# Kernel tuning notes

Measured on AMD Instinct MI355X. Metric: run time of the kernel, lower is better.

Reference implementation:

```python
import jax, jax.numpy as jnp
import numpy as np

# V:N:M sparsity config (n=2 kept of m=8 per vector-block; mask pattern [1,0,1,0,0,0,0,0])
M_BLK = 8
KEEP_OFFSETS = np.array([0, 2], dtype=np.int32)  # positions kept in each m-block
B, S, D_IN, D_OUT = 2, 8192, 4096, 4096
K_KEPT = D_IN // M_BLK * len(KEEP_OFFSETS)  # 1024


def _keep_idx():
    # column indices of the surviving weight entries (same for every output row)
    blocks = np.arange(D_IN // M_BLK, dtype=np.int32)[:, None] * M_BLK  # [D_IN/M,1]
    return jnp.asarray((blocks + KEEP_OFFSETS[None, :]).reshape(-1))   # [K_KEPT]


def setup_inputs() -> dict:
    key = jax.random.key(0)
    k1, k2, k3 = jax.random.split(key, 3)
    x = jax.random.normal(k1, (B, S, D_IN), dtype=jnp.float32)
    values = jax.random.normal(k2, (D_OUT, K_KEPT), dtype=jnp.float32) * 0.02
    bias = jax.random.normal(k3, (D_OUT,), dtype=jnp.float32) * 0.02
    return {"x": x, "values": values, "bias": bias}


def reference(x, values, bias):
    # Sparse SpMM: gather kept input features, dense GEMM with compressed values.
    # Equivalent to x @ (masked dense W).T + bias, without materializing W.
    keep = _keep_idx()               # [K_KEPT] int32, constant metadata
    xg = x[..., keep]                # [B,S,K_KEPT]
    out = jnp.einsum('bsk,nk->bsn', xg, values) + bias  # [B,S,D_OUT]
    return out
```

## Files before the change

### kernel.cpp

```cpp
#include <hip/hip_runtime.h>
#include <hip/hip_bf16.h>


#define M_TOTAL 16384
#define DIN     4096
#define KDIM    1024
#define NDIM    4096

typedef unsigned short u16;
typedef unsigned int   u32;
typedef __bf16 bf16x8 __attribute__((ext_vector_type(8)));
typedef float  f32x4  __attribute__((ext_vector_type(4)));

typedef const void __attribute__((address_space(1)))* gp_t;
typedef void __attribute__((address_space(3)))*       lp_t;

__device__ __forceinline__ u16 f2bf(float f) {
    u32 u = __float_as_uint(f);
    u += 0x7FFFu + ((u >> 16) & 1u);
    return (u16)(u >> 16);
}
__device__ __forceinline__ u32 pack2(float a, float b) {
    return (u32)f2bf(a) | ((u32)f2bf(b) << 16);
}

__global__ void prep_kernel(const float* __restrict__ x, uint2* __restrict__ xg2,
                            const float* __restrict__ vals, uint4* __restrict__ vb4) {
    const int tid = threadIdx.x;
    if (blockIdx.x < 4096) {
        int i = blockIdx.x * 256 + tid;
        const int stride = 4096 * 256;
#pragma unroll
        for (int it = 0; it < 4; ++it, i += stride) {
            const f32x4* p = (const f32x4*)(x + (size_t)i * 16);
            f32x4 f0 = __builtin_nontemporal_load(p);
            f32x4 f1 = __builtin_nontemporal_load(p + 2);
            xg2[i] = make_uint2(pack2(f0.x, f0.z), pack2(f1.x, f1.z));
        }
    } else {
        const int i = (blockIdx.x - 4096) * 256 + tid;
        const f32x4* p = (const f32x4*)(vals + (size_t)i * 8);
        f32x4 a = __builtin_nontemporal_load(p);
        f32x4 b = __builtin_nontemporal_load(p + 1);
        vb4[i] = make_uint4(pack2(a.x, a.y), pack2(a.z, a.w),
                            pack2(b.x, b.y), pack2(b.z, b.w));
    }
}


#define LDSA(d, kh) (((d) * 2 + (kh)) * 16384)
#define LDSB(d, kh) (65536 + ((d) * 2 + (kh)) * 16384)

#define LOADA(d, kh, mh) { _Pragma("unroll") \
    for (int m_ = 0; m_ < 4; ++m_) \
        af[m_] = *(const bf16x8*)(lds + LDSA(d, kh) + (wr * 8 + (mh) * 4 + m_) * 1024 + fl_off); }

#define LOADB(d, kh) { _Pragma("unroll") \
    for (int n_ = 0; n_ < 4; ++n_) \
        bfr[n_] = *(const bf16x8*)(lds + LDSB(d, kh) + (wc * 4 + n_) * 1024 + fl_off); }

#define MFMA16(mh) { \
    __builtin_amdgcn_s_setprio(1); \
    _Pragma("unroll") for (int m_ = 0; m_ < 4; ++m_) \
    _Pragma("unroll") for (int n_ = 0; n_ < 4; ++n_) \
        acc[(mh) * 4 + m_][n_] = __builtin_amdgcn_mfma_f32_16x16x32_bf16( \
            af[m_], bfr[n_], acc[(mh) * 4 + m_][n_], 0, 0, 0); \
    __builtin_amdgcn_s_setprio(0); }

#define BAR() __builtin_amdgcn_s_barrier()
#define VMCNT6() asm volatile("s_waitcnt vmcnt(6)" ::: "memory")

__global__ __launch_bounds__(512, 2) void gemm_kernel(
    const u16* __restrict__ A, const u16* __restrict__ Bv,
    const float* __restrict__ bias, float* __restrict__ C)
{
    __shared__ __align__(1024) char lds[131072];

    const int tid  = threadIdx.x;
    const int lane = tid & 63;
    const int wid  = tid >> 6;
    const int wr   = wid >> 2;
    const int wc   = wid & 3;
    const int lrow = lane & 15;
    const int lg   = lane >> 4;

    const int bb   = blockIdx.x;
    const int btm0 = (bb & 7) * 8 + (bb >> 7);
    const int btn  = (bb >> 3) & 15;

    const int st_r0 = wid * 16 + (lane >> 2);
    const int st_ck = ((lane & 3) * 8) ^ ((lane & 32) >> 1);
    const u16* A0  = A  + (size_t)(btm0 * 256 + st_r0) * KDIM + st_ck;
    const u16* Bs0 = Bv + (size_t)(btn  * 256 + st_r0) * KDIM + st_ck;
    const int dst0 = tid * 16;

    const int fl_off = lrow * 64 + ((lg * 16) ^ (((lrow >> 3) & 1) << 5));

    auto STAGE = [&](const u16* as_, int s) {
        const int kt = s >> 2, j = s & 3;
        const int d = kt & 1, kh = (j >> 1) & 1;
        const int ko = kt * 64 + kh * 32;
        const u16* src = (j & 1) ? Bs0 : as_;
        const int base = ((j & 1) ? 65536 : 0) + (d * 2 + kh) * 16384;
        __builtin_amdgcn_global_load_lds((gp_t)(src + ko),
            (lp_t)(lds + base + dst0), 16, 0, 0);
        __builtin_amdgcn_global_load_lds((gp_t)(src + 128 * KDIM + ko),
            (lp_t)(lds + base + 8192 + dst0), 16, 0, 0);
    };

    const int c_col0 = btn * 256 + wc * 64 + lrow;
    float bvr[4];
#pragma unroll
    for (int n = 0; n < 4; ++n) bvr[n] = bias[c_col0 + n * 16];

    f32x4 acc[8][4] = {};
    bf16x8 af[4], bfr[4];

    STAGE(A0, 0); STAGE(A0, 1); STAGE(A0, 2); STAGE(A0, 3);
    STAGE(A0, 4); STAGE(A0, 5); STAGE(A0, 6);
    VMCNT6();
    BAR();

#pragma unroll 1
    for (int r = 0; r < 4; ++r) {
        const u16* Ar = A0 + (size_t)r * 512 * KDIM;
        const u16* An = (r < 3) ? (Ar + 512 * KDIM) : Ar;

#pragma unroll 1
        for (int t = 0; t < 7; ++t) {
            const int s0 = 8 * t + 7;
            LOADB(0, 0); LOADA(0, 0, 0); STAGE(Ar, s0);     BAR(); MFMA16(0); BAR();
            LOADA(0, 0, 1);              STAGE(Ar, s0 + 1); BAR(); MFMA16(1); BAR();
            LOADB(0, 1); LOADA(0, 1, 0); STAGE(Ar, s0 + 2); BAR(); MFMA16(0); BAR();
            LOADA(0, 1, 1);              STAGE(Ar, s0 + 3); BAR(); MFMA16(1);
            VMCNT6(); BAR();
            LOADB(1, 0); LOADA(1, 0, 0); STAGE(Ar, s0 + 4); BAR(); MFMA16(0); BAR();
            LOADA(1, 0, 1);              STAGE(Ar, s0 + 5); BAR(); MFMA16(1); BAR();
            LOADB(1, 1); LOADA(1, 1, 0); STAGE(Ar, s0 + 6); BAR(); MFMA16(0); BAR();
            LOADA(1, 1, 1);              STAGE(Ar, s0 + 7); BAR(); MFMA16(1);
            VMCNT6(); BAR();
        }
        LOADB(0, 0); LOADA(0, 0, 0); STAGE(Ar, 63); BAR(); MFMA16(0); BAR();
        LOADA(0, 0, 1);              STAGE(An, 0);  BAR(); MFMA16(1); BAR();
        LOADB(0, 1); LOADA(0, 1, 0); STAGE(An, 1);  BAR(); MFMA16(0); BAR();
        LOADA(0, 1, 1);              STAGE(An, 2);  BAR(); MFMA16(1);
        VMCNT6(); BAR();
        LOADB(1, 0); LOADA(1, 0, 0); STAGE(An, 3);  BAR(); MFMA16(0); BAR();
        LOADA(1, 0, 1);              STAGE(An, 4);  BAR(); MFMA16(1); BAR();
        LOADB(1, 1); LOADA(1, 1, 0); STAGE(An, 5);  BAR(); MFMA16(0); BAR();
        LOADA(1, 1, 1);              STAGE(An, 6);  BAR(); MFMA16(1);
        VMCNT6(); BAR();

        const int c_row0 = (btm0 + 2 * r) * 256 + wr * 128 + lg * 4;
#pragma unroll
        for (int mi = 0; mi < 8; ++mi) {
            const int row = c_row0 + (mi >> 2) * 64 + (mi & 3) * 16;
#pragma unroll
            for (int n = 0; n < 4; ++n) {
#pragma unroll
                for (int j = 0; j < 4; ++j)
                    __builtin_nontemporal_store(acc[mi][n][j] + bvr[n],
                        &C[(size_t)(row + j) * NDIM + c_col0 + n * 16]);
                acc[mi][n] = (f32x4){0.f, 0.f, 0.f, 0.f};
            }
        }
    }
}

extern "C" void kernel_launch(void* const* d_in, const int* in_sizes, int n_in,
                              void* d_out, int out_size, void* d_ws, size_t ws_size,
                              hipStream_t stream) {
    const float* x      = (const float*)d_in[0];
    const float* values = (const float*)d_in[1];
    const float* bias   = (const float*)d_in[2];
    float* out = (float*)d_out;

    u16* xg = (u16*)d_ws;
    u16* vb = (u16*)((char*)d_ws + ((size_t)32 << 20));

    prep_kernel<<<6144, 256, 0, stream>>>(x, (uint2*)xg, values, (uint4*)vb);
    gemm_kernel<<<256, 512, 0, stream>>>(xg, vb, bias, out);
}
```

Measured before the change: 212.4 us.

## Restructure GEMM main loop into per-phase wait/barrier pipeline

Reorganizes the GEMM K-loop so each phase first waits on outstanding global-to-LDS loads (vmcnt 10) and then hits a single barrier before issuing the next stage and the LDS fragment reads. This replaces the previous pattern of two barriers per phase plus a vmcnt(6) every four phases, aiming to cut barrier count and keep more loads in flight. The first iteration after the epilogue uses a no-op wait because the next-tile prefetch was already issued. It adds risk of LDS read/write races if the wait counts or buffer reuse distance are wrong.

```diff
diff --git a/kernel.cpp b/kernel.cpp
--- a/kernel.cpp
+++ b/kernel.cpp
@@ -68,7 +68,30 @@
     __builtin_amdgcn_s_setprio(0); }
 
 #define BAR() __builtin_amdgcn_s_barrier()
-#define VMCNT6() asm volatile("s_waitcnt vmcnt(6)" ::: "memory")
+#define VMCNT10() asm volatile("s_waitcnt vmcnt(10)" ::: "memory")
+#define VMCNT63() asm volatile("s_waitcnt vmcnt(63)" ::: "memory")
+
+#define PH(W, STG, LDS_, mh) { W; BAR(); STG; LDS_; MFMA16(mh); }
+
+#define ITER(As_, Sb, W) { \
+  PH(W, STAGE(As_, (Sb) + 0), LOADB(0,0); LOADA(0,0,0), 0) \
+  PH(W, STAGE(As_, (Sb) + 1), LOADA(0,0,1),             1) \
+  PH(W, STAGE(As_, (Sb) + 2), LOADB(0,1); LOADA(0,1,0), 0) \
+  PH(W, STAGE(As_, (Sb) + 3), LOADA(0,1,1),             1) \
+  PH(W, STAGE(As_, (Sb) + 4), LOADB(1,0); LOADA(1,0,0), 0) \
+  PH(W, STAGE(As_, (Sb) + 5), LOADA(1,0,1),             1) \
+  PH(W, STAGE(As_, (Sb) + 6), LOADB(1,1); LOADA(1,1,0), 0) \
+  PH(W, STAGE(As_, (Sb) + 7), LOADA(1,1,1),             1) }
+
+#define TAIL_ITER(Ar_, An_) { \
+  PH(VMCNT10(), STAGE(Ar_, 63), LOADB(0,0); LOADA(0,0,0), 0) \
+  PH(VMCNT10(), STAGE(An_, 0),  LOADA(0,0,1),             1) \
+  PH(VMCNT10(), STAGE(An_, 1),  LOADB(0,1); LOADA(0,1,0), 0) \
+  PH(VMCNT10(), STAGE(An_, 2),  LOADA(0,1,1),             1) \
+  PH(VMCNT10(), STAGE(An_, 3),  LOADB(1,0); LOADA(1,0,0), 0) \
+  PH(VMCNT10(), STAGE(An_, 4),  LOADA(1,0,1),             1) \
+  PH(VMCNT10(), STAGE(An_, 5),  LOADB(1,1); LOADA(1,1,0), 0) \
+  PH(VMCNT10(), STAGE(An_, 6),  LOADA(1,1,1),             1) }
 
 __global__ __launch_bounds__(512, 2) void gemm_kernel(
     const u16* __restrict__ A, const u16* __restrict__ Bv,
@@ -118,38 +141,20 @@
 
     STAGE(A0, 0); STAGE(A0, 1); STAGE(A0, 2); STAGE(A0, 3);
     STAGE(A0, 4); STAGE(A0, 5); STAGE(A0, 6);
-    VMCNT6();
-    BAR();
 
 #pragma unroll 1
     for (int r = 0; r < 4; ++r) {
         const u16* Ar = A0 + (size_t)r * 512 * KDIM;
         const u16* An = (r < 3) ? (Ar + 512 * KDIM) : Ar;
 
+        if (r == 0) { ITER(Ar, 7, VMCNT10()) }
+        else        { ITER(Ar, 7, VMCNT63()) }
+
 #pragma unroll 1
-        for (int t = 0; t < 7; ++t) {
-            const int s0 = 8 * t + 7;
-            LOADB(0, 0); LOADA(0, 0, 0); STAGE(Ar, s0);     BAR(); MFMA16(0); BAR();
-            LOADA(0, 0, 1);              STAGE(Ar, s0 + 1); BAR(); MFMA16(1); BAR();
-            LOADB(0, 1); LOADA(0, 1, 0); STAGE(Ar, s0 + 2); BAR(); MFMA16(0); BAR();
-            LOADA(0, 1, 1);              STAGE(Ar, s0 + 3); BAR(); MFMA16(1);
-            VMCNT6(); BAR();
-            LOADB(1, 0); LOADA(1, 0, 0); STAGE(Ar, s0 + 4); BAR(); MFMA16(0); BAR();
-            LOADA(1, 0, 1);              STAGE(Ar, s0 + 5); BAR(); MFMA16(1); BAR();
-            LOADB(1, 1); LOADA(1, 1, 0); STAGE(Ar, s0 + 6); BAR(); MFMA16(0); BAR();
-            LOADA(1, 1, 1);              STAGE(Ar, s0 + 7); BAR(); MFMA16(1);
-            VMCNT6(); BAR();
+        for (int u = 1; u < 7; ++u) {
+            ITER(Ar, 8 * u + 7, VMCNT10())
         }
-        LOADB(0, 0); LOADA(0, 0, 0); STAGE(Ar, 63); BAR(); MFMA16(0); BAR();
-        LOADA(0, 0, 1);              STAGE(An, 0);  BAR(); MFMA16(1); BAR();
-        LOADB(0, 1); LOADA(0, 1, 0); STAGE(An, 1);  BAR(); MFMA16(0); BAR();
-        LOADA(0, 1, 1);              STAGE(An, 2);  BAR(); MFMA16(1);
-        VMCNT6(); BAR();
-        LOADB(1, 0); LOADA(1, 0, 0); STAGE(An, 3);  BAR(); MFMA16(0); BAR();
-        LOADA(1, 0, 1);              STAGE(An, 4);  BAR(); MFMA16(1); BAR();
-        LOADB(1, 1); LOADA(1, 1, 0); STAGE(An, 5);  BAR(); MFMA16(0); BAR();
-        LOADA(1, 1, 1);              STAGE(An, 6);  BAR(); MFMA16(1);
-        VMCNT6(); BAR();
+        TAIL_ITER(Ar, An)
 
         const int c_row0 = (btm0 + 2 * r) * 256 + wr * 128 + lg * 4;
 #pragma unroll
```

Result: slower. 226.6 us (+6.6%).

## Double-buffer LDS fragments and retile blocks into 2x2 output tile groups

Applied to the files above, without the earlier changes.

Register fragments are now double-buffered (afA/afB, bfrA/bfrB), so the LDS reads for the next MFMA phase are issued before the current MFMAs. This removes one barrier per phase and lets LDS latency overlap matrix math. Each block also walks a 2x2 group of 256x256 output tiles instead of four M tiles sharing one N tile, which changes operand reuse in L2. The trade-offs are higher register pressure and vmcnt accounting that must stay exactly right across tile transitions.

```diff
diff --git a/kernel.cpp b/kernel.cpp
--- a/kernel.cpp
+++ b/kernel.cpp
@@ -51,24 +51,37 @@
 #define LDSA(d, kh) (((d) * 2 + (kh)) * 16384)
 #define LDSB(d, kh) (65536 + ((d) * 2 + (kh)) * 16384)
 
-#define LOADA(d, kh, mh) { _Pragma("unroll") \
+#define LA(d, kh, mh, AF) { _Pragma("unroll") \
     for (int m_ = 0; m_ < 4; ++m_) \
-        af[m_] = *(const bf16x8*)(lds + LDSA(d, kh) + (wr * 8 + (mh) * 4 + m_) * 1024 + fl_off); }
+        AF[m_] = *(const bf16x8*)(lds + LDSA(d, kh) + (wr * 8 + (mh) * 4 + m_) * 1024 + fl_off); }
 
-#define LOADB(d, kh) { _Pragma("unroll") \
+#define LB(d, kh, BF) { _Pragma("unroll") \
     for (int n_ = 0; n_ < 4; ++n_) \
-        bfr[n_] = *(const bf16x8*)(lds + LDSB(d, kh) + (wc * 4 + n_) * 1024 + fl_off); }
+        BF[n_] = *(const bf16x8*)(lds + LDSB(d, kh) + (wc * 4 + n_) * 1024 + fl_off); }
 
-#define MFMA16(mh) { \
+#define MFMA16(mh, AF, BF) { \
     __builtin_amdgcn_s_setprio(1); \
     _Pragma("unroll") for (int m_ = 0; m_ < 4; ++m_) \
     _Pragma("unroll") for (int n_ = 0; n_ < 4; ++n_) \
         acc[(mh) * 4 + m_][n_] = __builtin_amdgcn_mfma_f32_16x16x32_bf16( \
-            af[m_], bfr[n_], acc[(mh) * 4 + m_][n_], 0, 0, 0); \
+            AF[m_], BF[n_], acc[(mh) * 4 + m_][n_], 0, 0, 0); \
     __builtin_amdgcn_s_setprio(0); }
 
 #define BAR() __builtin_amdgcn_s_barrier()
-#define VMCNT6() asm volatile("s_waitcnt vmcnt(6)" ::: "memory")
+#define VM8  asm volatile("s_waitcnt vmcnt(8)"  ::: "memory");
+#define VM63 asm volatile("s_waitcnt vmcnt(63)" ::: "memory");
+
+#define PHASE(W, S_, RD, MH, AF, BF) { W BAR(); STAGE(S_); RD MFMA16(MH, AF, BF); }
+
+#define ITER2(W1, W2, S0) { \
+  PHASE(W1, (S0)+0, LA(0,0,1,afB),                0, afA, bfrA) \
+  PHASE(W1, (S0)+1, LB(0,1,bfrB) LA(0,1,0,afA),   1, afB, bfrA) \
+  PHASE(W1, (S0)+2, LA(0,1,1,afB),                0, afA, bfrB) \
+  PHASE(W1, (S0)+3, LB(1,0,bfrA) LA(1,0,0,afA),   1, afB, bfrB) \
+  PHASE(W2, (S0)+4, LA(1,0,1,afB),                0, afA, bfrA) \
+  PHASE(W2, (S0)+5, LB(1,1,bfrB) LA(1,1,0,afA),   1, afB, bfrA) \
+  PHASE(W2, (S0)+6, LA(1,1,1,afB),                0, afA, bfrB) \
+  PHASE(W2, (S0)+7, LB(0,0,bfrA) LA(0,0,0,afA),   1, afB, bfrB) }
 
 __global__ __launch_bounds__(512, 2) void gemm_kernel(
     const u16* __restrict__ A, const u16* __restrict__ Bv,
@@ -84,74 +97,70 @@
     const int lrow = lane & 15;
     const int lg   = lane >> 4;
 
-    const int bb   = blockIdx.x;
-    const int btm0 = (bb & 7) * 8 + (bb >> 7);
-    const int btn  = (bb >> 3) & 15;
+    const int bb  = blockIdx.x;
+    const int c   = bb & 7;
+    const int idx = bb >> 3;
+    const int im  = idx & 3;
+    const int in_ = idx >> 2;
 
     const int st_r0 = wid * 16 + (lane >> 2);
     const int st_ck = ((lane & 3) * 8) ^ ((lane & 32) >> 1);
-    const u16* A0  = A  + (size_t)(btm0 * 256 + st_r0) * KDIM + st_ck;
-    const u16* Bs0 = Bv + (size_t)(btn  * 256 + st_r0) * KDIM + st_ck;
     const int dst0 = tid * 16;
 
     const int fl_off = lrow * 64 + ((lg * 16) ^ (((lrow >> 3) & 1) << 5));
 
-    auto STAGE = [&](const u16* as_, int s) {
-        const int kt = s >> 2, j = s & 3;
-        const int d = kt & 1, kh = (j >> 1) & 1;
-        const int ko = kt * 64 + kh * 32;
-        const u16* src = (j & 1) ? Bs0 : as_;
-        const int base = ((j & 1) ? 65536 : 0) + (d * 2 + kh) * 16384;
+    auto PA = [&](int r) {
+        return A + (size_t)((c * 8 + im * 2 + (r >> 1)) * 256 + st_r0) * KDIM + st_ck;
+    };
+    auto PB = [&](int r) {
+        return Bv + (size_t)((in_ * 2 + (r & 1)) * 256 + st_r0) * KDIM + st_ck;
+    };
+
+    const u16* curA = PA(0);
+    const u16* curB = PB(0);
+    const u16* nxtA = curA;
+    const u16* nxtB = curB;
+
+    auto STAGE = [&](int s) {
+        const int ss = s & 63;
+        const u16* sa = (s >= 64) ? nxtA : curA;
+        const u16* sb = (s >= 64) ? nxtB : curB;
+        const int tt = ss >> 2, kh = (ss >> 1) & 1, isB = ss & 1, d = tt & 1;
+        const int ko = tt * 64 + kh * 32;
+        const u16* src = isB ? sb : sa;
+        const int base = isB * 65536 + (d * 2 + kh) * 16384;
         __builtin_amdgcn_global_load_lds((gp_t)(src + ko),
             (lp_t)(lds + base + dst0), 16, 0, 0);
         __builtin_amdgcn_global_load_lds((gp_t)(src + 128 * KDIM + ko),
             (lp_t)(lds + base + 8192 + dst0), 16, 0, 0);
     };
 
-    const int c_col0 = btn * 256 + wc * 64 + lrow;
-    float bvr[4];
-#pragma unroll
-    for (int n = 0; n < 4; ++n) bvr[n] = bias[c_col0 + n * 16];
+    f32x4 acc[8][4] = {};
+    bf16x8 afA[4], afB[4], bfrA[4], bfrB[4];
 
-    f32x4 acc[8][4] = {};
-    bf16x8 af[4], bfr[4];
-
-    STAGE(A0, 0); STAGE(A0, 1); STAGE(A0, 2); STAGE(A0, 3);
-    STAGE(A0, 4); STAGE(A0, 5); STAGE(A0, 6);
-    VMCNT6();
+    STAGE(0); STAGE(1); STAGE(2); STAGE(3); STAGE(4); STAGE(5); STAGE(6);
+    asm volatile("s_waitcnt vmcnt(10)" ::: "memory");
     BAR();
+    LB(0, 0, bfrA) LA(0, 0, 0, afA)
 
 #pragma unroll 1
     for (int r = 0; r < 4; ++r) {
-        const u16* Ar = A0 + (size_t)r * 512 * KDIM;
-        const u16* An = (r < 3) ? (Ar + 512 * KDIM) : Ar;
+        nxtA = (r < 3) ? PA(r + 1) : curA;
+        nxtB = (r < 3) ? PB(r + 1) : curB;
+
+        if (r == 0) { ITER2(VM8, VM8, 7) }
+        else        { ITER2(VM63, VM8, 7) }
 
 #pragma unroll 1
-        for (int t = 0; t < 7; ++t) {
-            const int s0 = 8 * t + 7;
-            LOADB(0, 0); LOADA(0, 0, 0); STAGE(Ar, s0);     BAR(); MFMA16(0); BAR();
-            LOADA(0, 0, 1);              STAGE(Ar, s0 + 1); BAR(); MFMA16(1); BAR();
-            LOADB(0, 1); LOADA(0, 1, 0); STAGE(Ar, s0 + 2); BAR(); MFMA16(0); BAR();
-            LOADA(0, 1, 1);              STAGE(Ar, s0 + 3); BAR(); MFMA16(1);
-            VMCNT6(); BAR();
-            LOADB(1, 0); LOADA(1, 0, 0); STAGE(Ar, s0 + 4); BAR(); MFMA16(0); BAR();
-            LOADA(1, 0, 1);              STAGE(Ar, s0 + 5); BAR(); MFMA16(1); BAR();
-            LOADB(1, 1); LOADA(1, 1, 0); STAGE(Ar, s0 + 6); BAR(); MFMA16(0); BAR();
-            LOADA(1, 1, 1);              STAGE(Ar, s0 + 7); BAR(); MFMA16(1);
-            VMCNT6(); BAR();
+        for (int u = 1; u < 8; ++u) {
+            ITER2(VM8, VM8, 8 * u + 7)
         }
-        LOADB(0, 0); LOADA(0, 0, 0); STAGE(Ar, 63); BAR(); MFMA16(0); BAR();
-        LOADA(0, 0, 1);              STAGE(An, 0);  BAR(); MFMA16(1); BAR();
-        LOADB(0, 1); LOADA(0, 1, 0); STAGE(An, 1);  BAR(); MFMA16(0); BAR();
-        LOADA(0, 1, 1);              STAGE(An, 2);  BAR(); MFMA16(1);
-        VMCNT6(); BAR();
-        LOADB(1, 0); LOADA(1, 0, 0); STAGE(An, 3);  BAR(); MFMA16(0); BAR();
-        LOADA(1, 0, 1);              STAGE(An, 4);  BAR(); MFMA16(1); BAR();
-        LOADB(1, 1); LOADA(1, 1, 0); STAGE(An, 5);  BAR(); MFMA16(0); BAR();
-        LOADA(1, 1, 1);              STAGE(An, 6);  BAR(); MFMA16(1);
-        VMCNT6(); BAR();
 
-        const int c_row0 = (btm0 + 2 * r) * 256 + wr * 128 + lg * 4;
+        const int c_row0 = (c * 8 + im * 2 + (r >> 1)) * 256 + wr * 128 + lg * 4;
+        const int c_col0 = (in_ * 2 + (r & 1)) * 256 + wc * 64 + lrow;
+        float bvr[4];
+#pragma unroll
+        for (int n = 0; n < 4; ++n) bvr[n] = bias[c_col0 + n * 16];
 #pragma unroll
         for (int mi = 0; mi < 8; ++mi) {
             const int row = c_row0 + (mi >> 2) * 64 + (mi & 3) * 16;
@@ -164,6 +173,8 @@
                 acc[mi][n] = (f32x4){0.f, 0.f, 0.f, 0.f};
             }
         }
+        curA = nxtA;
+        curB = nxtB;
     }
 }
 
```

Result: slower. 264.0 us (+24.3%).

## Switch GEMM to one tile per block with finer-grained vmcnt pipelining

Applied to the files above, without the earlier changes.

The persistent 256-block kernel, which looped over four M-tiles per block, is replaced by 1024 blocks that each compute a single 256x256 tile, with an XCD-aware block swizzle. The LDS stage layout and the wait points are reorganised into per-stage vmcnt(10)/vmcnt(14) waits, so that wait-then-barrier comes before each LDS read. The MFMA operands are swapped so the accumulator layout is transposed, which lets the epilogue write 16-byte vector stores with vector bias loads instead of scalar nontemporal stores. The cost is a fresh pipeline prologue and drain in every block, and the output rows now go through normal cached stores.

```diff
diff --git a/kernel.cpp b/kernel.cpp
--- a/kernel.cpp
+++ b/kernel.cpp
@@ -48,8 +48,8 @@
 }
 
 
-#define LDSA(d, kh) (((d) * 2 + (kh)) * 16384)
-#define LDSB(d, kh) (65536 + ((d) * 2 + (kh)) * 16384)
+#define LDSA(d, kh) (((d) * 4 + 2 * (kh)) * 16384)
+#define LDSB(d, kh) (((d) * 4 + 2 * (kh) + 1) * 16384)
 
 #define LOADA(d, kh, mh) { _Pragma("unroll") \
     for (int m_ = 0; m_ < 4; ++m_) \
@@ -64,11 +64,12 @@
     _Pragma("unroll") for (int m_ = 0; m_ < 4; ++m_) \
     _Pragma("unroll") for (int n_ = 0; n_ < 4; ++n_) \
         acc[(mh) * 4 + m_][n_] = __builtin_amdgcn_mfma_f32_16x16x32_bf16( \
-            af[m_], bfr[n_], acc[(mh) * 4 + m_][n_], 0, 0, 0); \
+            bfr[n_], af[m_], acc[(mh) * 4 + m_][n_], 0, 0, 0); \
     __builtin_amdgcn_s_setprio(0); }
 
-#define BAR() __builtin_amdgcn_s_barrier()
-#define VMCNT6() asm volatile("s_waitcnt vmcnt(6)" ::: "memory")
+#define BAR()  __builtin_amdgcn_s_barrier()
+#define VM10() asm volatile("s_waitcnt vmcnt(10)" ::: "memory")
+#define VM14() asm volatile("s_waitcnt vmcnt(14)" ::: "memory")
 
 __global__ __launch_bounds__(512, 2) void gemm_kernel(
     const u16* __restrict__ A, const u16* __restrict__ Bv,
@@ -84,85 +85,63 @@
     const int lrow = lane & 15;
     const int lg   = lane >> 4;
 
-    const int bb   = blockIdx.x;
-    const int btm0 = (bb & 7) * 8 + (bb >> 7);
-    const int btn  = (bb >> 3) & 15;
+    const int b   = blockIdx.x;
+    const int swz = (b & 7) * 128 + (b >> 3);
+    const int btm = swz >> 4;
+    const int btn = swz & 15;
 
     const int st_r0 = wid * 16 + (lane >> 2);
     const int st_ck = ((lane & 3) * 8) ^ ((lane & 32) >> 1);
-    const u16* A0  = A  + (size_t)(btm0 * 256 + st_r0) * KDIM + st_ck;
-    const u16* Bs0 = Bv + (size_t)(btn  * 256 + st_r0) * KDIM + st_ck;
+    const u16* Ap = A  + (size_t)(btm * 256 + st_r0) * KDIM + st_ck;
+    const u16* Bp = Bv + (size_t)(btn * 256 + st_r0) * KDIM + st_ck;
     const int dst0 = tid * 16;
 
     const int fl_off = lrow * 64 + ((lg * 16) ^ (((lrow >> 3) & 1) << 5));
 
-    auto STAGE = [&](const u16* as_, int s) {
-        const int kt = s >> 2, j = s & 3;
-        const int d = kt & 1, kh = (j >> 1) & 1;
-        const int ko = kt * 64 + kh * 32;
-        const u16* src = (j & 1) ? Bs0 : as_;
-        const int base = ((j & 1) ? 65536 : 0) + (d * 2 + kh) * 16384;
+    auto STAGE = [&](int s) {
+        const int ss = (s < 64) ? s : s - 8;
+        const int tt = ss >> 2, kh = (ss >> 1) & 1, isB = ss & 1;
+        const int ko = tt * 64 + kh * 32;
+        const u16* src = isB ? Bp : Ap;
+        const int base = (ss & 7) * 16384;
         __builtin_amdgcn_global_load_lds((gp_t)(src + ko),
             (lp_t)(lds + base + dst0), 16, 0, 0);
         __builtin_amdgcn_global_load_lds((gp_t)(src + 128 * KDIM + ko),
             (lp_t)(lds + base + 8192 + dst0), 16, 0, 0);
     };
 
-    const int c_col0 = btn * 256 + wc * 64 + lrow;
-    float bvr[4];
-#pragma unroll
-    for (int n = 0; n < 4; ++n) bvr[n] = bias[c_col0 + n * 16];
-
     f32x4 acc[8][4] = {};
     bf16x8 af[4], bfr[4];
 
-    STAGE(A0, 0); STAGE(A0, 1); STAGE(A0, 2); STAGE(A0, 3);
-    STAGE(A0, 4); STAGE(A0, 5); STAGE(A0, 6);
-    VMCNT6();
-    BAR();
+    STAGE(0); STAGE(1); STAGE(2); STAGE(3); STAGE(4); STAGE(5); STAGE(6);
 
 #pragma unroll 1
-    for (int r = 0; r < 4; ++r) {
-        const u16* Ar = A0 + (size_t)r * 512 * KDIM;
-        const u16* An = (r < 3) ? (Ar + 512 * KDIM) : Ar;
+    for (int t = 0; t < 16; ++t) {
+        const int d = t & 1;
+        const int p = 4 * t;
+        VM10(); BAR(); LOADB(d, 0); LOADA(d, 0, 0); STAGE(p + 7);
+        BAR(); MFMA16(0);
+        VM14(); BAR(); LOADA(d, 0, 1); STAGE(p + 8);
+        BAR(); MFMA16(1);
+        VM10(); BAR(); LOADB(d, 1); LOADA(d, 1, 0); STAGE(p + 9);
+        BAR(); MFMA16(0);
+        VM14(); BAR(); LOADA(d, 1, 1); STAGE(p + 10);
+        BAR(); MFMA16(1);
+    }
 
-#pragma unroll 1
-        for (int t = 0; t < 7; ++t) {
-            const int s0 = 8 * t + 7;
-            LOADB(0, 0); LOADA(0, 0, 0); STAGE(Ar, s0);     BAR(); MFMA16(0); BAR();
-            LOADA(0, 0, 1);              STAGE(Ar, s0 + 1); BAR(); MFMA16(1); BAR();
-            LOADB(0, 1); LOADA(0, 1, 0); STAGE(Ar, s0 + 2); BAR(); MFMA16(0); BAR();
-            LOADA(0, 1, 1);              STAGE(Ar, s0 + 3); BAR(); MFMA16(1);
-            VMCNT6(); BAR();
-            LOADB(1, 0); LOADA(1, 0, 0); STAGE(Ar, s0 + 4); BAR(); MFMA16(0); BAR();
-            LOADA(1, 0, 1);              STAGE(Ar, s0 + 5); BAR(); MFMA16(1); BAR();
-            LOADB(1, 1); LOADA(1, 1, 0); STAGE(Ar, s0 + 6); BAR(); MFMA16(0); BAR();
-            LOADA(1, 1, 1);              STAGE(Ar, s0 + 7); BAR(); MFMA16(1);
-            VMCNT6(); BAR();
-        }
-        LOADB(0, 0); LOADA(0, 0, 0); STAGE(Ar, 63); BAR(); MFMA16(0); BAR();
-        LOADA(0, 0, 1);              STAGE(An, 0);  BAR(); MFMA16(1); BAR();
-        LOADB(0, 1); LOADA(0, 1, 0); STAGE(An, 1);  BAR(); MFMA16(0); BAR();
-        LOADA(0, 1, 1);              STAGE(An, 2);  BAR(); MFMA16(1);
-        VMCNT6(); BAR();
-        LOADB(1, 0); LOADA(1, 0, 0); STAGE(An, 3);  BAR(); MFMA16(0); BAR();
-        LOADA(1, 0, 1);              STAGE(An, 4);  BAR(); MFMA16(1); BAR();
-        LOADB(1, 1); LOADA(1, 1, 0); STAGE(An, 5);  BAR(); MFMA16(0); BAR();
-        LOADA(1, 1, 1);              STAGE(An, 6);  BAR(); MFMA16(1);
-        VMCNT6(); BAR();
-
-        const int c_row0 = (btm0 + 2 * r) * 256 + wr * 128 + lg * 4;
+    const int c_row0 = btm * 256 + wr * 128 + lrow;
+    const int c_col0 = btn * 256 + wc * 64 + lg * 4;
+    f32x4 bvr[4];
 #pragma unroll
-        for (int mi = 0; mi < 8; ++mi) {
-            const int row = c_row0 + (mi >> 2) * 64 + (mi & 3) * 16;
+    for (int n = 0; n < 4; ++n)
+        bvr[n] = *(const f32x4*)&bias[c_col0 + n * 16];
 #pragma unroll
-            for (int n = 0; n < 4; ++n) {
+    for (int mi = 0; mi < 8; ++mi) {
+        const int row = c_row0 + (mi >> 2) * 64 + (mi & 3) * 16;
 #pragma unroll
-                for (int j = 0; j < 4; ++j)
-                    __builtin_nontemporal_store(acc[mi][n][j] + bvr[n],
-                        &C[(size_t)(row + j) * NDIM + c_col0 + n * 16]);
-                acc[mi][n] = (f32x4){0.f, 0.f, 0.f, 0.f};
-            }
+        for (int n = 0; n < 4; ++n) {
+            f32x4 v = acc[mi][n] + bvr[n];
+            *(f32x4*)&C[(size_t)row * NDIM + c_col0 + n * 16] = v;
         }
     }
 }
@@ -179,5 +158,5 @@
     u16* vb = (u16*)((char*)d_ws + ((size_t)32 << 20));
 
     prep_kernel<<<6144, 256, 0, stream>>>(x, (uint2*)xg, values, (uint4*)vb);
-    gemm_kernel<<<256, 512, 0, stream>>>(xg, vb, bias, out);
+    gemm_kernel<<<1024, 512, 0, stream>>>(xg, vb, bias, out);
 }
```

Result: no change. 216.6 us (+2.0%).
